# Performance work log

Measured on AMD Instinct MI355X. Metric: run time of the kernel, lower is better.

Reference implementation:

```python
import jax, jax.numpy as jnp
import numpy as np

# Device / mapping constants (from iterator config in the original repo)
V_REF = 0.25
K_V = 2.0 * V_REF
G_MIN = 1e-5
G_MAX = 1e-3
N_AVG = 2.99
N_STD = 0.37
N_IN, N_OUT, BATCH = 1024, 512, 128


def setup_inputs() -> dict:
    key = jax.random.key(0)
    ks = jax.random.split(key, 6)
    x = jax.random.uniform(ks[0], (BATCH, N_IN), dtype=jnp.float32)
    stdv = 1.0 / np.sqrt(N_IN)
    w_pos = 0.5 + stdv * jax.random.normal(ks[1], (N_IN, N_OUT), dtype=jnp.float32)
    w_neg = 0.5 + stdv * jax.random.normal(ks[2], (N_IN, N_OUT), dtype=jnp.float32)
    b_pos = 0.5 * jnp.ones((N_OUT,), jnp.float32)
    b_neg = 0.5 * jnp.ones((N_OUT,), jnp.float32)
    # per-crosspoint I-V nonlinearity parameter n (n=2 means ohmic); clip below at 2
    n_devices = jnp.maximum(
        N_AVG + N_STD * jax.random.normal(ks[3], (N_IN + 1, 2 * N_OUT), dtype=jnp.float32),
        2.0,
    )
    return {"x": x, "w_pos": w_pos, "w_neg": w_neg, "b_pos": b_pos,
            "b_neg": b_neg, "n_devices": n_devices}


def reference(x, w_pos, w_neg, b_pos, b_neg, n_devices):
    B = x.shape[0]
    # append bias input of 1s -> [B, n_in+1]
    inputs = jnp.concatenate([x, jnp.ones((B, 1), x.dtype)], axis=1)
    # combined weights with bias row -> [n_in+1, n_out] each
    cw_pos = jnp.concatenate([w_pos, b_pos[None, :]], axis=0)
    cw_neg = jnp.concatenate([w_neg, b_neg[None, :]], axis=0)
    # interleave pos/neg columns -> [n_in+1, 2*n_out]
    combined = jnp.stack([cw_pos, cw_neg], axis=-1).reshape(cw_pos.shape[0], -1)
    # x -> V mapping
    V = K_V * inputs  # [B, n_in+1]
    # weight params -> conductances
    max_weight = jnp.max(jnp.abs(combined))
    k_G = (G_MAX - G_MIN) / max_weight
    G = k_G * jnp.abs(combined) + G_MIN  # [n_in+1, 2*n_out]
    # nonlinear I-V: I(V) = sign(V) * G*V_ref * (|V|/V_ref)^log2(n)
    exponent = jnp.log2(n_devices)          # [n_in+1, 2*n_out]
    sgn = jnp.sign(V)                       # [B, n_in+1]
    ratio = jnp.abs(V) / V_REF              # [B, n_in+1]
    I_ind = (sgn[:, :, None] * (G * V_REF)[None, :, :]
             * ratio[:, :, None] ** exponent[None, :, :])  # [B, n_in+1, 2*n_out]
    I = jnp.sum(I_ind, axis=1)              # [B, 2*n_out] (sum along bit lines)
    # differential pair currents -> output
    I_total = I[:, 0::2] - I[:, 1::2]       # [B, n_out]
    y = I_total / (K_V * k_G)
    return y
```

## Files before the change

### kernel.cpp

```cpp
#include <hip/hip_runtime.h>
#include <cstdint>
#include <cstddef>


#define B128 128
#define NIN  1024
#define NI   1025
#define NO   512
#define NJ   1024
#define GMIN 1.0e-5f
#define GSPAN (1.0e-3f - 1.0e-5f)
#define ZCH  8
#define CHUNK 128

__device__ __forceinline__ float flog2(float x) { return __builtin_amdgcn_logf(x); }
__device__ __forceinline__ float fexp2(float x) { return __builtin_amdgcn_exp2f(x); }

__global__ __launch_bounds__(1024) void k_prep(
    const float* __restrict__ x,
    const float* __restrict__ wp, const float* __restrict__ wn,
    const float* __restrict__ bp, const float* __restrict__ bn,
    float* __restrict__ LT, float* __restrict__ bmax, float* __restrict__ out)
{
    const int tid = blockIdx.x * 1024 + threadIdx.x;

    if (tid < B128 * NO) out[tid] = 0.0f;

    if (tid < NI * B128) {
        int i = tid >> 7, b = tid & 127;
        float xv = (i < NIN) ? x[b * NIN + i] : 1.0f;
        LT[tid] = 1.0f + flog2(xv);
    }

    float m = fmaxf(fmaxf(__builtin_fabsf(wp[tid]), __builtin_fabsf(wn[tid])),
                    fmaxf(__builtin_fabsf(wp[tid + 262144]), __builtin_fabsf(wn[tid + 262144])));
    if (tid < NO) m = fmaxf(m, fmaxf(__builtin_fabsf(bp[tid]), __builtin_fabsf(bn[tid])));

    __shared__ float red[16];
    #pragma unroll
    for (int off = 32; off > 0; off >>= 1) m = fmaxf(m, __shfl_down(m, off, 64));
    if ((threadIdx.x & 63) == 0) red[threadIdx.x >> 6] = m;
    __syncthreads();
    if (threadIdx.x < 16) {
        m = red[threadIdx.x];
        #pragma unroll
        for (int off = 8; off > 0; off >>= 1) m = fmaxf(m, __shfl_down(m, off, 16));
        if (threadIdx.x == 0) bmax[blockIdx.x] = m;
    }
}

__global__ __launch_bounds__(512) void k_main(
    const float* __restrict__ nd,
    const float* __restrict__ wp, const float* __restrict__ wn,
    const float* __restrict__ bp, const float* __restrict__ bn,
    const float* __restrict__ LT, const float* __restrict__ bmax,
    float* __restrict__ out)
{
    const int lane = threadIdx.x & 63;
    const int s    = __builtin_amdgcn_readfirstlane(threadIdx.x >> 6);
    const int o    = (blockIdx.x << 6) + lane;
    const int b0   = blockIdx.y << 4;

    float m = fmaxf(fmaxf(bmax[lane], bmax[lane + 64]),
                    fmaxf(bmax[lane + 128], bmax[lane + 192]));
    #pragma unroll
    for (int off = 32; off > 0; off >>= 1) m = fmaxf(m, __shfl_down(m, off, 64));
    const float maxw = __shfl(m, 0, 64);
    const float kG = GSPAN / maxw;
    const float C  = 0.5f * maxw / GSPAN;

    const int i0 = blockIdx.z * CHUNK + s;

    const float* pnd = nd + (size_t)i0 * NJ + 2 * o;
    const float* pwp = wp + (size_t)i0 * NO + o;
    const float* pwn = wn + (size_t)i0 * NO + o;
    const float* pL  = LT + (size_t)i0 * B128 + b0;

    float accp[16], accn[16];
    #pragma unroll
    for (int k = 0; k < 16; ++k) { accp[k] = 0.0f; accn[k] = 0.0f; }

    float2 nv = *(const float2*)pnd;
    float wvp = *pwp;
    float wvn = *pwn;
    float Lv[16];
    #pragma unroll
    for (int j = 0; j < 16; ++j) Lv[j] = pL[j];

    #pragma unroll 2
    for (int k = 0; k < 15; ++k) {
        pnd += 8 * NJ; pwp += 8 * NO; pwn += 8 * NO; pL += 8 * B128;
        float2 nv_n = *(const float2*)pnd;
        float wp_n = *pwp;
        float wn_n = *pwn;
        float Lv_n[16];
        #pragma unroll
        for (int j = 0; j < 16; ++j) Lv_n[j] = pL[j];

        const float Ep = flog2(nv.x);
        const float En = flog2(nv.y);
        const float Wp = flog2(__builtin_fmaf(kG, __builtin_fabsf(wvp), GMIN));
        const float Wn = flog2(__builtin_fmaf(kG, __builtin_fabsf(wvn), GMIN));

        #pragma unroll
        for (int j = 0; j < 16; ++j) {
            accp[j] += fexp2(__builtin_fmaf(Ep, Lv[j], Wp));
            accn[j] += fexp2(__builtin_fmaf(En, Lv[j], Wn));
        }

        nv = nv_n; wvp = wp_n; wvn = wn_n;
        #pragma unroll
        for (int j = 0; j < 16; ++j) Lv[j] = Lv_n[j];
    }

    {
        const float Ep = flog2(nv.x);
        const float En = flog2(nv.y);
        const float Wp = flog2(__builtin_fmaf(kG, __builtin_fabsf(wvp), GMIN));
        const float Wn = flog2(__builtin_fmaf(kG, __builtin_fabsf(wvn), GMIN));
        #pragma unroll
        for (int j = 0; j < 16; ++j) {
            accp[j] += fexp2(__builtin_fmaf(Ep, Lv[j], Wp));
            accn[j] += fexp2(__builtin_fmaf(En, Lv[j], Wn));
        }
    }

    __shared__ float lds[8 * 64 * 17];
    {
        const int base = ((threadIdx.x >> 6) * 64 + lane) * 17;
        #pragma unroll
        for (int j = 0; j < 16; ++j) lds[base + j] = accp[j] - accn[j];
    }
    __syncthreads();

    {
        const int l = threadIdx.x & 63;
        #pragma unroll
        for (int r = 0; r < 2; ++r) {
            const int b = (threadIdx.x >> 6) + (r << 3);
            float sum = 0.0f;
            #pragma unroll
            for (int w = 0; w < 8; ++w) sum += lds[(w * 64 + l) * 17 + b];

            if (blockIdx.z == 0) {
                const int oo = (blockIdx.x << 6) + l;
                const float2 nb = *(const float2*)(nd + (size_t)NIN * NJ + 2 * oo);
                const float gp = __builtin_fmaf(kG, __builtin_fabsf(bp[oo]), GMIN);
                const float gn = __builtin_fmaf(kG, __builtin_fabsf(bn[oo]), GMIN);
                sum += nb.x * gp - nb.y * gn;
            }
            unsafeAtomicAdd(out + (size_t)(b0 + b) * NO + (blockIdx.x << 6) + l, C * sum);
        }
    }
}

extern "C" void kernel_launch(void* const* d_in, const int* in_sizes, int n_in,
                              void* d_out, int out_size, void* d_ws, size_t ws_size,
                              hipStream_t stream)
{
    const float* x  = (const float*)d_in[0];
    const float* wp = (const float*)d_in[1];
    const float* wn = (const float*)d_in[2];
    const float* bp = (const float*)d_in[3];
    const float* bn = (const float*)d_in[4];
    const float* nd = (const float*)d_in[5];
    float* out = (float*)d_out;

    unsigned char* ws = (unsigned char*)d_ws;
    float* bmax = (float*)ws;
    float* LT   = (float*)(ws + 4096);

    k_prep<<<256, 1024, 0, stream>>>(x, wp, wn, bp, bn, LT, bmax, out);
    k_main<<<dim3(8, 8, ZCH), 512, 0, stream>>>(nd, wp, wn, bp, bn, LT, bmax, out);
}
```

Measured before the change: 90.07 us.

## Precompute log2 of device exponents and stage input logs in shared memory

Measured after the change: 90.51 us. No clear change (+0.5%).

```diff
diff --git a/kernel.cpp b/kernel.cpp
--- a/kernel.cpp
+++ b/kernel.cpp
@@ -17,10 +17,11 @@
 __device__ __forceinline__ float fexp2(float x) { return __builtin_amdgcn_exp2f(x); }
 
 __global__ __launch_bounds__(1024) void k_prep(
-    const float* __restrict__ x,
+    const float* __restrict__ x, const float* __restrict__ nd,
     const float* __restrict__ wp, const float* __restrict__ wn,
     const float* __restrict__ bp, const float* __restrict__ bn,
-    float* __restrict__ LT, float* __restrict__ bmax, float* __restrict__ out)
+    float* __restrict__ LT, float* __restrict__ Elog,
+    float* __restrict__ bmax, float* __restrict__ out)
 {
     const int tid = blockIdx.x * 1024 + threadIdx.x;
 
@@ -31,6 +32,9 @@
         float xv = (i < NIN) ? x[b * NIN + i] : 1.0f;
         LT[tid] = 1.0f + flog2(xv);
     }
+
+    for (int t = tid; t < NI * NJ; t += 262144)
+        Elog[t] = flog2(nd[t]);
 
     float m = fmaxf(fmaxf(__builtin_fabsf(wp[tid]), __builtin_fabsf(wn[tid])),
                     fmaxf(__builtin_fabsf(wp[tid + 262144]), __builtin_fabsf(wn[tid + 262144])));
@@ -53,13 +57,24 @@
     const float* __restrict__ nd,
     const float* __restrict__ wp, const float* __restrict__ wn,
     const float* __restrict__ bp, const float* __restrict__ bn,
-    const float* __restrict__ LT, const float* __restrict__ bmax,
-    float* __restrict__ out)
+    const float* __restrict__ LT, const float* __restrict__ Elog,
+    const float* __restrict__ bmax, float* __restrict__ out)
 {
     const int lane = threadIdx.x & 63;
-    const int s    = __builtin_amdgcn_readfirstlane(threadIdx.x >> 6);
+    const int s    = threadIdx.x >> 6;
     const int o    = (blockIdx.x << 6) + lane;
     const int b0   = blockIdx.y << 4;
+    const int i0   = blockIdx.z * CHUNK;
+
+    __shared__ float lds[8 * 64 * 17];
+    float* tile = lds;
+
+    {
+        const int t = threadIdx.x;
+        const int row = t >> 2, c4 = (t & 3) << 2;
+        const float4 v = *(const float4*)(LT + (size_t)(i0 + row) * B128 + b0 + c4);
+        *(float4*)(tile + row * 16 + c4) = v;
+    }
 
     float m = fmaxf(fmaxf(bmax[lane], bmax[lane + 64]),
                     fmaxf(bmax[lane + 128], bmax[lane + 192]));
@@ -69,65 +84,67 @@
     const float kG = GSPAN / maxw;
     const float C  = 0.5f * maxw / GSPAN;
 
-    const int i0 = blockIdx.z * CHUNK + s;
+    __syncthreads();
 
-    const float* pnd = nd + (size_t)i0 * NJ + 2 * o;
-    const float* pwp = wp + (size_t)i0 * NO + o;
-    const float* pwn = wn + (size_t)i0 * NO + o;
-    const float* pL  = LT + (size_t)i0 * B128 + b0;
+    const float* pEl = Elog + (size_t)(i0 + s) * NJ + 2 * o;
+    const float* pwp = wp + (size_t)(i0 + s) * NO + o;
+    const float* pwn = wn + (size_t)(i0 + s) * NO + o;
 
     float accp[16], accn[16];
     #pragma unroll
     for (int k = 0; k < 16; ++k) { accp[k] = 0.0f; accn[k] = 0.0f; }
 
-    float2 nv = *(const float2*)pnd;
+    float2 el = *(const float2*)pEl;
     float wvp = *pwp;
     float wvn = *pwn;
-    float Lv[16];
-    #pragma unroll
-    for (int j = 0; j < 16; ++j) Lv[j] = pL[j];
 
     #pragma unroll 2
     for (int k = 0; k < 15; ++k) {
-        pnd += 8 * NJ; pwp += 8 * NO; pwn += 8 * NO; pL += 8 * B128;
-        float2 nv_n = *(const float2*)pnd;
-        float wp_n = *pwp;
-        float wn_n = *pwn;
-        float Lv_n[16];
-        #pragma unroll
-        for (int j = 0; j < 16; ++j) Lv_n[j] = pL[j];
+        pEl += 8 * NJ; pwp += 8 * NO; pwn += 8 * NO;
+        const float2 el_n = *(const float2*)pEl;
+        const float wp_n = *pwp;
+        const float wn_n = *pwn;
 
-        const float Ep = flog2(nv.x);
-        const float En = flog2(nv.y);
-        const float Wp = flog2(__builtin_fmaf(kG, __builtin_fabsf(wvp), GMIN));
-        const float Wn = flog2(__builtin_fmaf(kG, __builtin_fabsf(wvn), GMIN));
+        const float gp = __builtin_fmaf(kG, __builtin_fabsf(wvp), GMIN);
+        const float gn = __builtin_fmaf(kG, __builtin_fabsf(wvn), GMIN);
 
+        const float* trow = tile + (s + 8 * k) * 16;
+        const float4 La = *(const float4*)(trow);
+        const float4 Lb = *(const float4*)(trow + 4);
+        const float4 Lc = *(const float4*)(trow + 8);
+        const float4 Ld = *(const float4*)(trow + 12);
+        const float Lv[16] = {La.x, La.y, La.z, La.w, Lb.x, Lb.y, Lb.z, Lb.w,
+                              Lc.x, Lc.y, Lc.z, Lc.w, Ld.x, Ld.y, Ld.z, Ld.w};
         #pragma unroll
         for (int j = 0; j < 16; ++j) {
-            accp[j] += fexp2(__builtin_fmaf(Ep, Lv[j], Wp));
-            accn[j] += fexp2(__builtin_fmaf(En, Lv[j], Wn));
+            accp[j] = __builtin_fmaf(gp, fexp2(el.x * Lv[j]), accp[j]);
+            accn[j] = __builtin_fmaf(gn, fexp2(el.y * Lv[j]), accn[j]);
         }
 
-        nv = nv_n; wvp = wp_n; wvn = wn_n;
-        #pragma unroll
-        for (int j = 0; j < 16; ++j) Lv[j] = Lv_n[j];
+        el = el_n; wvp = wp_n; wvn = wn_n;
     }
 
     {
-        const float Ep = flog2(nv.x);
-        const float En = flog2(nv.y);
-        const float Wp = flog2(__builtin_fmaf(kG, __builtin_fabsf(wvp), GMIN));
-        const float Wn = flog2(__builtin_fmaf(kG, __builtin_fabsf(wvn), GMIN));
+        const float gp = __builtin_fmaf(kG, __builtin_fabsf(wvp), GMIN);
+        const float gn = __builtin_fmaf(kG, __builtin_fabsf(wvn), GMIN);
+        const float* trow = tile + (s + 8 * 15) * 16;
+        const float4 La = *(const float4*)(trow);
+        const float4 Lb = *(const float4*)(trow + 4);
+        const float4 Lc = *(const float4*)(trow + 8);
+        const float4 Ld = *(const float4*)(trow + 12);
+        const float Lv[16] = {La.x, La.y, La.z, La.w, Lb.x, Lb.y, Lb.z, Lb.w,
+                              Lc.x, Lc.y, Lc.z, Lc.w, Ld.x, Ld.y, Ld.z, Ld.w};
         #pragma unroll
         for (int j = 0; j < 16; ++j) {
-            accp[j] += fexp2(__builtin_fmaf(Ep, Lv[j], Wp));
-            accn[j] += fexp2(__builtin_fmaf(En, Lv[j], Wn));
+            accp[j] = __builtin_fmaf(gp, fexp2(el.x * Lv[j]), accp[j]);
+            accn[j] = __builtin_fmaf(gn, fexp2(el.y * Lv[j]), accn[j]);
         }
     }
 
-    __shared__ float lds[8 * 64 * 17];
+    __syncthreads();
+
     {
-        const int base = ((threadIdx.x >> 6) * 64 + lane) * 17;
+        const int base = (s * 64 + lane) * 17;
         #pragma unroll
         for (int j = 0; j < 16; ++j) lds[base + j] = accp[j] - accn[j];
     }
@@ -169,7 +186,8 @@
     unsigned char* ws = (unsigned char*)d_ws;
     float* bmax = (float*)ws;
     float* LT   = (float*)(ws + 4096);
+    float* Elog = (float*)(ws + 4096 + 525056);
 
-    k_prep<<<256, 1024, 0, stream>>>(x, wp, wn, bp, bn, LT, bmax, out);
-    k_main<<<dim3(8, 8, ZCH), 512, 0, stream>>>(nd, wp, wn, bp, bn, LT, bmax, out);
+    k_prep<<<256, 1024, 0, stream>>>(x, nd, wp, wn, bp, bn, LT, Elog, bmax, out);
+    k_main<<<dim3(8, 8, ZCH), 512, 0, stream>>>(nd, wp, wn, bp, bn, LT, Elog, bmax, out);
 }
```
